# Kernel optimization log

Hardware: AMD Instinct MI355X
Metric: run time of the kernel (lower is better)

Reference implementation:

```python
import jax, jax.numpy as jnp
import numpy as np

B, T, F_DIM, HID, CH = 16, 4096, 47, 64, 256  # batch, frames, feature_dim, hidden_feature_dim, num_channels


def setup_inputs() -> dict:
    key = jax.random.key(0)
    ks = jax.random.split(key, 8)
    s = 0.08  # weight scale
    return {
        "features": jax.random.normal(ks[0], (B, T, F_DIM), jnp.float32),
        # conv1: Conv1d(47, 64, k=1) -> pointwise linear, torch weight (out,in,1) squeezed
        "W1": jax.random.normal(ks[1], (HID, F_DIM), jnp.float32) * s,
        "b1": jnp.zeros((HID,), jnp.float32),
        # conv2: Conv1d(256, 256, k=2), torch weight (out, in, k)
        "W2": jax.random.normal(ks[2], (CH, 4 * HID, 2), jnp.float32) * s,
        "b2": jnp.zeros((CH,), jnp.float32),
        # tconv: ConvTranspose1d(256, 256, k=4, stride=4), torch weight (in, out, k)
        "Wt": jax.random.normal(ks[3], (CH, CH, 4), jnp.float32) * s,
        "bt": jnp.zeros((CH,), jnp.float32),
        # GRU(256, 256), torch layout: (3*H, in) with gate order [r, z, n]
        "W_ih": jax.random.normal(ks[4], (3 * CH, CH), jnp.float32) * s,
        "W_hh": jax.random.normal(ks[5], (3 * CH, CH), jnp.float32) * s,
        "b_ih": jnp.zeros((3 * CH,), jnp.float32),
        "b_hh": jnp.zeros((3 * CH,), jnp.float32),
    }


def reference(features, W1, b1, W2, b2, Wt, bt, W_ih, W_hh, b_ih, b_hh):
    b, t = features.shape[0], features.shape[1]
    ch = Wt.shape[1]
    # conv1 (k=1) == pointwise linear + tanh: (B,T,47) -> (B,T,64)
    c = jnp.tanh(jnp.einsum('btf,hf->bth', features, W1) + b1)
    # group 4 frames: (B, T/4, 256)
    c = c.reshape(b, t // 4, -1)
    # conv2 k=2 with left pad 1 (causal): y[t] = W2[..0] x[t-1] + W2[..1] x[t]
    cp = jnp.pad(c, ((0, 0), (1, 0), (0, 0)))
    c = jnp.tanh(jnp.einsum('bti,oi->bto', cp[:, :-1], W2[:, :, 0])
                 + jnp.einsum('bti,oi->bto', cp[:, 1:], W2[:, :, 1]) + b2)
    # tconv: stride-4 transpose conv, k=4 -> each frame emits 4 steps
    c = jnp.tanh(jnp.einsum('bti,iok->btko', c, Wt) + bt)  # (B, T/4, 4, CH)
    c = c.reshape(b, t, ch)
    # GRU (torch semantics, gate order r,z,n); precompute input projections
    gates_x = jnp.einsum('btc,gc->btg', c, W_ih) + b_ih  # (B,T,3CH)

    def step(h, gx):
        gh = h @ W_hh.T + b_hh
        xr, xz, xn = jnp.split(gx, 3, axis=-1)
        hr, hz, hn = jnp.split(gh, 3, axis=-1)
        r = jax.nn.sigmoid(xr + hr)
        z = jax.nn.sigmoid(xz + hz)
        n = jnp.tanh(xn + r * hn)
        h = (1 - z) * n + z * h
        return h, h

    h0 = jnp.zeros((b, ch), features.dtype)
    _, hs = jax.lax.scan(step, h0, jnp.swapaxes(gates_x, 0, 1))  # (T,B,CH)
    return jnp.swapaxes(hs, 0, 1)  # (B,T,CH)
```

## Files before the change

### kernel.cpp

```cpp
#include <hip/hip_runtime.h>
#include <hip/hip_bf16.h>
#include <stdint.h>

#define B_   16
#define T_   4096
#define F_   47
#define HID_ 64
#define CH_  256
#define TG_  1024
#define G3_  768

using bf16x8 = __attribute__((ext_vector_type(8))) short;
using f32x4  = __attribute__((ext_vector_type(4))) float;
using f16x8  = __attribute__((ext_vector_type(8))) _Float16;
using h2     = __attribute__((ext_vector_type(2))) _Float16;

__device__ __forceinline__ short f2bf(float f) {
    union { float f; uint32_t u; } v; v.f = f;
    uint32_t u = v.u;
    uint32_t r = (u + 0x7fffu + ((u >> 16) & 1u)) >> 16;
    return (short)r;
}
__device__ __forceinline__ float bf2f(short s) {
    union { uint32_t u; float f; } v; v.u = ((uint32_t)(uint16_t)s) << 16;
    return v.f;
}
__device__ __forceinline__ float fast_tanh(float x) {
    float e = __expf(2.f * x);
    return 1.f - 2.f / (e + 1.f);
}
__device__ __forceinline__ float fast_sigmoid(float x) {
    return 1.f / (1.f + __expf(-x));
}

#if __has_builtin(__builtin_amdgcn_fdot2)
#define FDOT2(a, b, c) __builtin_amdgcn_fdot2((a), (b), (c), false)
#else
__device__ __forceinline__ float fdot2_emul(h2 a, h2 b, float c) {
    return c + (float)a[0] * (float)b[0] + (float)a[1] * (float)b[1];
}
#define FDOT2(a, b, c) fdot2_emul((a), (b), (c))
#endif

template <int CTRL>
__device__ __forceinline__ float dpp_add(float x) {
    union { float f; int i; } a, b;
    a.f = x;
    b.i = __builtin_amdgcn_update_dpp(0, a.i, CTRL, 0xf, 0xf, true);
    return x + b.f;
}

#if __has_builtin(__builtin_amdgcn_global_load_lds)
#define HAS_GLL 1
__device__ __forceinline__ void gl_lds16(const void* g, void* l) {
    __builtin_amdgcn_global_load_lds(
        (const __attribute__((address_space(1))) uint32_t*)g,
        (__attribute__((address_space(3))) uint32_t*)l, 16, 0, 0);
}
#else
#define HAS_GLL 0
#endif

__global__ __launch_bounds__(256) void k1_conv1(const float* __restrict__ feat,
        const float* __restrict__ W1, const float* __restrict__ b1,
        short* __restrict__ c1) {
    __shared__ float sW[47 * 64];
    __shared__ float sF[4 * 47];
    int tid = threadIdx.x;
    int b = blockIdx.x >> 10, t0 = (blockIdx.x & 1023) * 4;
    if (tid < 188) sF[tid] = feat[((size_t)b * T_ + t0) * 47 + tid];
    for (int i = tid; i < 47 * 64; i += 256) {
        int f = i >> 6, h = i & 63;
        sW[i] = W1[h * 47 + f];
    }
    __syncthreads();
    int fr = tid >> 6, h = tid & 63;
    float acc = b1[h];
    #pragma unroll
    for (int f = 0; f < 47; ++f)
        acc += sF[fr * 47 + f] * sW[f * 64 + h];
    c1[((size_t)b * T_ + t0 + fr) * 64 + h] = f2bf(fast_tanh(acc));
}

__global__ __launch_bounds__(256) void k_prep(const float* __restrict__ W2,
        const float* __restrict__ Wt, const float* __restrict__ Wih_f,
        short* __restrict__ W2t, short* __restrict__ Wtt, short* __restrict__ Wih) {
    int idx = blockIdx.x * 256 + threadIdx.x;
    if (idx < 256 * 512) {
        int o = idx >> 9, i = idx & 511, d = i >> 8, jj = i & 255;
        W2t[idx] = f2bf(W2[(size_t)o * 512 + jj * 2 + d]);
    }
    {
        int n = idx >> 8, ic = idx & 255, o = n & 255, kp = n >> 8;
        Wtt[idx] = f2bf(Wt[(size_t)ic * 1024 + o * 4 + kp]);
    }
    if (idx < G3_ * CH_)
        Wih[idx] = f2bf(Wih_f[idx]);
}

__global__ __launch_bounds__(256) void k2_conv2(const short* __restrict__ c1,
        const short* __restrict__ W2t, const float* __restrict__ b2,
        short* __restrict__ y2) {
    int tid = threadIdx.x, w = tid >> 6, l = tid & 63;
    int lane16 = l & 15, quad = l >> 4;
    int mt = blockIdx.x * 4 + w;
    int row = mt * 16 + lane16;
    int tg = row & 1023;
    const short* Arow = c1 + (size_t)row * 256 - 256;
    bf16x8 zero8 = {0,0,0,0,0,0,0,0};
    bf16x8 af[16];
    #pragma unroll
    for (int kt = 0; kt < 16; ++kt) {
        int i0 = kt * 32 + quad * 8;
        bool masked = (tg == 0) && (kt < 8);
        const short* p = masked ? c1 : (Arow + i0);
        bf16x8 v = *(const bf16x8*)p;
        af[kt] = masked ? zero8 : v;
    }
    #pragma unroll
    for (int nt = 0; nt < 16; ++nt) {
        int n = nt * 16 + lane16;
        f32x4 acc = {0.f, 0.f, 0.f, 0.f};
        const short* Brow = W2t + (size_t)n * 512 + quad * 8;
        #pragma unroll
        for (int kt = 0; kt < 16; ++kt) {
            bf16x8 bf = *(const bf16x8*)(Brow + kt * 32);
            acc = __builtin_amdgcn_mfma_f32_16x16x32_bf16(af[kt], bf, acc, 0, 0, 0);
        }
        float bias = b2[n];
        #pragma unroll
        for (int r = 0; r < 4; ++r) {
            int mrow = mt * 16 + quad * 4 + r;
            y2[(size_t)mrow * 256 + n] = f2bf(fast_tanh(acc[r] + bias));
        }
    }
}

__global__ __launch_bounds__(256) void k3a_tconv(const short* __restrict__ y2,
        const short* __restrict__ Wtt, const float* __restrict__ bt,
        short* __restrict__ c3) {
    int tid = threadIdx.x, w = tid >> 6, l = tid & 63;
    int lane16 = l & 15, quad = l >> 4;
    int mt = blockIdx.x;
    int row = mt * 16 + lane16;
    const short* Arow = y2 + (size_t)row * 256 + quad * 8;
    bf16x8 af[8];
    #pragma unroll
    for (int kt = 0; kt < 8; ++kt) af[kt] = *(const bf16x8*)(Arow + kt * 32);
    #pragma unroll
    for (int nt2 = 0; nt2 < 16; ++nt2) {
        int n = (w * 16 + nt2) * 16 + lane16;
        f32x4 acc = {0.f, 0.f, 0.f, 0.f};
        const short* Brow = Wtt + (size_t)n * 256 + quad * 8;
        #pragma unroll
        for (int kt = 0; kt < 8; ++kt) {
            bf16x8 bf = *(const bf16x8*)(Brow + kt * 32);
            acc = __builtin_amdgcn_mfma_f32_16x16x32_bf16(af[kt], bf, acc, 0, 0, 0);
        }
        int kp = n >> 8, o = n & 255;
        float bias = bt[o];
        #pragma unroll
        for (int r = 0; r < 4; ++r) {
            int mrow = mt * 16 + quad * 4 + r;
            int bb = mrow >> 10, tgg = mrow & 1023;
            c3[(((size_t)bb * TG_ + tgg) * 4 + kp) * 256 + o] =
                f2bf(fast_tanh(acc[r] + bias));
        }
    }
}

__global__ __launch_bounds__(256) void k3b_xproj(const short* __restrict__ c3,
        const short* __restrict__ Wih, const float* __restrict__ b_ih,
        short* __restrict__ gates) {
    int tid = threadIdx.x, w = tid >> 6, l = tid & 63;
    int lane16 = l & 15, quad = l >> 4;
    int mt = blockIdx.x;
    int row = mt * 16 + lane16;
    const short* Arow = c3 + (size_t)row * 256 + quad * 8;
    bf16x8 af[8];
    #pragma unroll
    for (int kt = 0; kt < 8; ++kt) af[kt] = *(const bf16x8*)(Arow + kt * 32);
    #pragma unroll
    for (int nt2 = 0; nt2 < 12; ++nt2) {
        int n = (w * 12 + nt2) * 16 + lane16;
        f32x4 acc = {0.f, 0.f, 0.f, 0.f};
        const short* Brow = Wih + (size_t)n * 256 + quad * 8;
        #pragma unroll
        for (int kt = 0; kt < 8; ++kt) {
            bf16x8 bf = *(const bf16x8*)(Brow + kt * 32);
            acc = __builtin_amdgcn_mfma_f32_16x16x32_bf16(af[kt], bf, acc, 0, 0, 0);
        }
        float bias = b_ih[n];
        #pragma unroll
        for (int r = 0; r < 4; ++r) {
            int mrow = mt * 16 + quad * 4 + r;
            gates[(size_t)mrow * G3_ + n] = f2bf(acc[r] + bias);
        }
    }
}

__global__ __launch_bounds__(1024) void k4_gru_dot2(const float* __restrict__ W_hh,
        const float* __restrict__ b_hh, const short* __restrict__ gates,
        float* __restrict__ out) {
    __shared__ __align__(16) short gxb[2][8][G3_];
    __shared__ __align__(16) float part[G3_];
    __shared__ __align__(16) float ob[8 * 256];
    __shared__ __align__(16) short hq_s[2][4 * 72];

    int tid = threadIdx.x, l = tid & 63, w = tid >> 6;
    int q = tid & 3, n0 = tid >> 2;
    int b = blockIdx.x;

    h2 wreg[3][32];
    #pragma unroll
    for (int k = 0; k < 3; ++k) {
        const float2* row = (const float2*)(W_hh + ((size_t)(n0 + k * 256)) * 256 + q * 64);
        #pragma unroll
        for (int j = 0; j < 32; ++j) {
            float2 v = row[j];
            h2 p; p[0] = (_Float16)v.x; p[1] = (_Float16)v.y;
            wreg[k][j] = p;
        }
    }

    float h_reg = 0.f, bhr = 0.f, bhz = 0.f, bhn = 0.f;
    if (tid < 256) {
        bhr = b_hh[tid]; bhz = b_hh[256 + tid]; bhn = b_hh[512 + tid];
    }
    if (tid < 288) hq_s[0][tid] = 0;

    const short* gbase = gates + (size_t)b * T_ * G3_;
    const char* gbytes = (const char*)gbase;

#if HAS_GLL
    if (w < 12) {
        char* dst = (char*)&gxb[0][0][0];
        gl_lds16(gbytes + w * 1024 + l * 16, dst + w * 1024);
    }
#else
    {
        const uint32_t* g32 = (const uint32_t*)gbytes;
        uint32_t* d = (uint32_t*)&gxb[0][0][0];
        #pragma unroll
        for (int i = 0; i < 3; ++i) d[tid + i * 1024] = g32[tid + i * 1024];
    }
#endif
    __syncthreads();

    float* outb = out + (size_t)b * T_ * CH_;
    for (int s = 0; s < T_; ++s) {
        bool grp0 = ((s & 7) == 0) && (s + 8 < T_);
#if HAS_GLL
        if (grp0 && w < 12) {
            const char* src = gbytes + (size_t)(s + 8) * 1536;
            char* dst = (char*)&gxb[((s >> 3) + 1) & 1][0][0];
            gl_lds16(src + w * 1024 + l * 16, dst + w * 1024);
        }
#else
        uint32_t pf[3];
        if (grp0) {
            const uint32_t* src = (const uint32_t*)(gbytes + (size_t)(s + 8) * 1536);
            #pragma unroll
            for (int i = 0; i < 3; ++i) pf[i] = src[tid + i * 1024];
        }
#endif

        float acc0 = 0.f, acc1 = 0.f, acc2 = 0.f;
        const short* hb = &hq_s[s & 1][q * 72];
        #pragma unroll
        for (int g2 = 0; g2 < 8; ++g2) {
            f16x8 v = *(const f16x8*)(hb + g2 * 8);
            #pragma unroll
            for (int p2 = 0; p2 < 4; ++p2) {
                h2 hv; hv[0] = v[p2 * 2]; hv[1] = v[p2 * 2 + 1];
                acc0 = FDOT2(wreg[0][g2 * 4 + p2], hv, acc0);
                acc1 = FDOT2(wreg[1][g2 * 4 + p2], hv, acc1);
                acc2 = FDOT2(wreg[2][g2 * 4 + p2], hv, acc2);
            }
        }

        acc0 = dpp_add<0xB1>(acc0); acc0 = dpp_add<0x4E>(acc0);
        acc1 = dpp_add<0xB1>(acc1); acc1 = dpp_add<0x4E>(acc1);
        acc2 = dpp_add<0xB1>(acc2); acc2 = dpp_add<0x4E>(acc2);
        if (q == 0) {
            part[n0]       = acc0;
            part[256 + n0] = acc1;
            part[512 + n0] = acc2;
        }
        __syncthreads();

#if !HAS_GLL
        if (grp0) {
            uint32_t* d = (uint32_t*)&gxb[((s >> 3) + 1) & 1][0][0];
            #pragma unroll
            for (int i = 0; i < 3; ++i) d[tid + i * 1024] = pf[i];
        }
#endif
        if (tid < 256) {
            const short* gx = &gxb[(s >> 3) & 1][s & 7][0];
            float gr = part[tid];
            float gz = part[256 + tid];
            float gn = part[512 + tid];
            float xr = bf2f(gx[tid]), xz = bf2f(gx[256 + tid]), xn = bf2f(gx[512 + tid]);
            float r = fast_sigmoid(xr + gr + bhr);
            float z = fast_sigmoid(xz + gz + bhz);
            float nn = fast_tanh(xn + r * (gn + bhn));
            h_reg = (1.f - z) * nn + z * h_reg;
            union { _Float16 f; short u; } cv; cv.f = (_Float16)h_reg;
            hq_s[(s + 1) & 1][(tid >> 6) * 72 + (tid & 63)] = cv.u;
            ob[(s & 7) * 256 + tid] = h_reg;
        }
        __syncthreads();

        if ((s & 7) == 7 && tid < 512) {
            f32x4 v = *(const f32x4*)&ob[tid * 4];
            *(f32x4*)&outb[(size_t)(s - 7 + (tid >> 6)) * 256 + (tid & 63) * 4] = v;
        }
    }
}

extern "C" void kernel_launch(void* const* d_in, const int* in_sizes, int n_in,
                              void* d_out, int out_size, void* d_ws, size_t ws_size,
                              hipStream_t stream) {
    const float* feat  = (const float*)d_in[0];
    const float* W1    = (const float*)d_in[1];
    const float* b1    = (const float*)d_in[2];
    const float* W2    = (const float*)d_in[3];
    const float* b2    = (const float*)d_in[4];
    const float* Wt    = (const float*)d_in[5];
    const float* bt    = (const float*)d_in[6];
    const float* Wih_f = (const float*)d_in[7];
    const float* Whh   = (const float*)d_in[8];
    const float* bih   = (const float*)d_in[9];
    const float* bhh   = (const float*)d_in[10];
    float* out = (float*)d_out;

    char* ws = (char*)d_ws;
    short* c3    = (short*)(ws);
    short* c1    = (short*)(ws);
    short* gates = (short*)(ws + 33554432);
    short* y2    = (short*)(ws + 33554432);
    short* W2t   = (short*)(ws + 134217728);
    short* Wtt   = (short*)(ws + 134217728 + 262144);
    short* Wih   = (short*)(ws + 134217728 + 262144 + 524288);

    k1_conv1   <<<16384, 256, 0, stream>>>(feat, W1, b1, c1);
    k_prep     <<<1024, 256, 0, stream>>>(W2, Wt, Wih_f, W2t, Wtt, Wih);
    k2_conv2   <<<256,  256, 0, stream>>>(c1, W2t, b2, y2);
    k3a_tconv  <<<1024, 256, 0, stream>>>(y2, Wtt, bt, c3);
    k3b_xproj  <<<4096, 256, 0, stream>>>(c3, Wih, bih, gates);
    k4_gru_dot2<<<16,   1024, 0, stream>>>(Whh, bhh, gates, out);
}
```

Before: 5.822 ms.

## Fuse GRU gate update into dot-product lanes and drop one barrier per step

```diff
diff --git a/kernel.cpp b/kernel.cpp
--- a/kernel.cpp
+++ b/kernel.cpp
@@ -199,13 +199,12 @@
     }
 }
 
-__global__ __launch_bounds__(1024) void k4_gru_dot2(const float* __restrict__ W_hh,
+__global__ __launch_bounds__(1024, 4) void k4_gru_dot2(const float* __restrict__ W_hh,
         const float* __restrict__ b_hh, const short* __restrict__ gates,
         float* __restrict__ out) {
     __shared__ __align__(16) short gxb[2][8][G3_];
-    __shared__ __align__(16) float part[G3_];
-    __shared__ __align__(16) float ob[8 * 256];
-    __shared__ __align__(16) short hq_s[2][4 * 72];
+    __shared__ __align__(16) float ob[2][8 * 256];
+    __shared__ __align__(16) _Float16 hq_s[2][256];
 
     int tid = threadIdx.x, l = tid & 63, w = tid >> 6;
     int q = tid & 3, n0 = tid >> 2;
@@ -223,11 +222,9 @@
         }
     }
 
-    float h_reg = 0.f, bhr = 0.f, bhz = 0.f, bhn = 0.f;
-    if (tid < 256) {
-        bhr = b_hh[tid]; bhz = b_hh[256 + tid]; bhn = b_hh[512 + tid];
-    }
-    if (tid < 288) hq_s[0][tid] = 0;
+    float bhr = b_hh[n0], bhz = b_hh[256 + n0], bhn = b_hh[512 + n0];
+    float h_reg = 0.f;
+    if (tid < 256) hq_s[0][tid] = (_Float16)0.f;
 
     const short* gbase = gates + (size_t)b * T_ * G3_;
     const char* gbytes = (const char*)gbase;
@@ -257,22 +254,23 @@
             gl_lds16(src + w * 1024 + l * 16, dst + w * 1024);
         }
 #else
-        uint32_t pf[3];
         if (grp0) {
             const uint32_t* src = (const uint32_t*)(gbytes + (size_t)(s + 8) * 1536);
+            uint32_t* d = (uint32_t*)&gxb[((s >> 3) + 1) & 1][0][0];
             #pragma unroll
-            for (int i = 0; i < 3; ++i) pf[i] = src[tid + i * 1024];
+            for (int i = 0; i < 3; ++i) d[tid + i * 1024] = src[tid + i * 1024];
         }
 #endif
 
         float acc0 = 0.f, acc1 = 0.f, acc2 = 0.f;
-        const short* hb = &hq_s[s & 1][q * 72];
+        const _Float16* hb = &hq_s[s & 1][q * 64];
         #pragma unroll
         for (int g2 = 0; g2 < 8; ++g2) {
-            f16x8 v = *(const f16x8*)(hb + g2 * 8);
+            union { f16x8 v8; h2 p[4]; } hc;
+            hc.v8 = *(const f16x8*)(hb + g2 * 8);
             #pragma unroll
             for (int p2 = 0; p2 < 4; ++p2) {
-                h2 hv; hv[0] = v[p2 * 2]; hv[1] = v[p2 * 2 + 1];
+                h2 hv = hc.p[p2];
                 acc0 = FDOT2(wreg[0][g2 * 4 + p2], hv, acc0);
                 acc1 = FDOT2(wreg[1][g2 * 4 + p2], hv, acc1);
                 acc2 = FDOT2(wreg[2][g2 * 4 + p2], hv, acc2);
@@ -282,38 +280,21 @@
         acc0 = dpp_add<0xB1>(acc0); acc0 = dpp_add<0x4E>(acc0);
         acc1 = dpp_add<0xB1>(acc1); acc1 = dpp_add<0x4E>(acc1);
         acc2 = dpp_add<0xB1>(acc2); acc2 = dpp_add<0x4E>(acc2);
+
         if (q == 0) {
-            part[n0]       = acc0;
-            part[256 + n0] = acc1;
-            part[512 + n0] = acc2;
+            const short* gx = &gxb[(s >> 3) & 1][s & 7][0];
+            float xr = bf2f(gx[n0]), xz = bf2f(gx[256 + n0]), xn = bf2f(gx[512 + n0]);
+            float r = fast_sigmoid(xr + acc0 + bhr);
+            float z = fast_sigmoid(xz + acc1 + bhz);
+            float nn = fast_tanh(xn + r * (acc2 + bhn));
+            h_reg = (1.f - z) * nn + z * h_reg;
+            hq_s[(s + 1) & 1][n0] = (_Float16)h_reg;
+            ob[(s >> 3) & 1][(s & 7) * 256 + n0] = h_reg;
         }
         __syncthreads();
 
-#if !HAS_GLL
-        if (grp0) {
-            uint32_t* d = (uint32_t*)&gxb[((s >> 3) + 1) & 1][0][0];
-            #pragma unroll
-            for (int i = 0; i < 3; ++i) d[tid + i * 1024] = pf[i];
-        }
-#endif
-        if (tid < 256) {
-            const short* gx = &gxb[(s >> 3) & 1][s & 7][0];
-            float gr = part[tid];
-            float gz = part[256 + tid];
-            float gn = part[512 + tid];
-            float xr = bf2f(gx[tid]), xz = bf2f(gx[256 + tid]), xn = bf2f(gx[512 + tid]);
-            float r = fast_sigmoid(xr + gr + bhr);
-            float z = fast_sigmoid(xz + gz + bhz);
-            float nn = fast_tanh(xn + r * (gn + bhn));
-            h_reg = (1.f - z) * nn + z * h_reg;
-            union { _Float16 f; short u; } cv; cv.f = (_Float16)h_reg;
-            hq_s[(s + 1) & 1][(tid >> 6) * 72 + (tid & 63)] = cv.u;
-            ob[(s & 7) * 256 + tid] = h_reg;
-        }
-        __syncthreads();
-
         if ((s & 7) == 7 && tid < 512) {
-            f32x4 v = *(const f32x4*)&ob[tid * 4];
+            f32x4 v = *(const f32x4*)&ob[(s >> 3) & 1][tid * 4];
             *(f32x4*)&outb[(size_t)(s - 7 + (tid >> 6)) * 256 + (tid & 63) * 4] = v;
         }
     }
```

Result: slower. 6.715 ms (+15.4%).
